# Kernel tuning notes

Measured on AMD Instinct MI355X. Metric: run time of the kernel, lower is better.

## Reference

```python
import jax, jax.numpy as jnp
import numpy as np

N = 50000      # nodes
D = 256        # input_features
K = 64         # hiddens (per-head out dim)
H = 8          # nheads
O = 64         # outputs
E = 1600000    # edges
ALPHA = 0.2    # leaky-relu negative slope


def setup_inputs() -> dict:
    key = jax.random.key(0)
    ks = jax.random.split(key, 8)
    x = jax.random.normal(ks[0], (N, D), dtype=jnp.float32)
    edges = jax.random.randint(ks[1], (2, E), 0, N, dtype=jnp.int64)
    layer_W = jax.random.normal(ks[2], (D, D), dtype=jnp.float32) * (1.0 / np.sqrt(D))
    layer_b = jnp.zeros((D,), dtype=jnp.float32)
    heads_W = jax.random.normal(ks[3], (H, D, K), dtype=jnp.float32) * (1.0 / np.sqrt(D))
    heads_a = jax.random.normal(ks[4], (H, 2 * K), dtype=jnp.float32) * 0.1
    end_W = jax.random.normal(ks[5], (H * K, O), dtype=jnp.float32) * (1.0 / np.sqrt(H * K))
    end_a = jax.random.normal(ks[6], (2 * O,), dtype=jnp.float32) * 0.1
    return {"x": x, "edges": edges, "layer_W": layer_W, "layer_b": layer_b,
            "heads_W": heads_W, "heads_a": heads_a, "end_W": end_W, "end_a": end_a}


def _gat_layer(x, W, a, src, dst):
    # x: [N, Din], W: [Din, Dout], a: [2*Dout]
    h = x @ W                                    # [N, Dout]
    k = h.shape[1]
    # a . [h_src || h_dst] == (h @ a_src)[src] + (h @ a_dst)[dst]  (cheap: project then gather scalars)
    s = (h @ a[:k])[src] + (h @ a[k:])[dst]      # [E]
    e = jax.nn.leaky_relu(s, ALPHA)
    # numerically-stable segment softmax over edges grouped by destination node
    m = jax.ops.segment_max(e, dst, num_segments=N)        # [N]
    w = jnp.exp(e - m[dst])                                # [E]
    denom = jax.ops.segment_sum(w, dst, num_segments=N)    # [N]
    attn = w / (denom[dst] + 1e-16)                        # [E]
    out = jax.ops.segment_sum(attn[:, None] * h[src], dst, num_segments=N)  # [N, Dout]
    return jax.nn.elu(out)


def reference(x, edges, layer_W, layer_b, heads_W, heads_a, end_W, end_a):
    src, dst = edges[0], edges[1]
    x = x @ layer_W + layer_b                    # nn.Linear(input_features, input_features)
    # multi-head sparse attention, concat over heads -> [N, H*K]
    hcat = jnp.concatenate(
        [_gat_layer(x, heads_W[i], heads_a[i], src, dst) for i in range(H)], axis=1)
    out = _gat_layer(hcat, end_W, end_a, src, dst)  # [N, O]
    return jax.nn.softmax(out, axis=1)
```

## Files before the change

kernel.cpp:

```cpp
#include <hip/hip_runtime.h>
#include <hip/hip_fp16.h>
#include <math.h>

#define NN 50000
#define DD 256
#define KK 64
#define HH 8
#define OO 64
#define EE 1600000
#define LRELU_ALPHA 0.2f
#define HK 512
#define NX 640
#define N3 80

typedef __attribute__((ext_vector_type(8))) short short8;
typedef __attribute__((ext_vector_type(4))) float floatx4;
typedef __attribute__((ext_vector_type(4))) unsigned int uintx4;

__device__ inline void bsplit(float f, unsigned short& h, unsigned short& l) {
    unsigned u = __float_as_uint(f);
    h = (unsigned short)(u >> 16);
    float fh = __uint_as_float(u & 0xffff0000u);
    l = (unsigned short)(__float_as_uint(f - fh) >> 16);
}

__device__ inline void fmamix2(float& a0, float& a1, unsigned int pk, float w) {
    asm("v_fma_mix_f32 %0, %2, %3, %0 op_sel:[0,0,0] op_sel_hi:[1,0,0]\n\t"
        "v_fma_mix_f32 %1, %2, %3, %1 op_sel:[1,0,0] op_sel_hi:[1,0,0]"
        : "+v"(a0), "+v"(a1)
        : "v"(pk), "v"(w));
}

__global__ void pack_heads_kernel(const float* __restrict__ hw, float* __restrict__ Bp) {
    int t = blockIdx.x * 256 + threadIdx.x;
    if (t >= HH * DD * KK) return;
    int h = t >> 14;
    int r = t & 16383;
    int d = r >> 6;
    int k = r & 63;
    Bp[d * HK + h * KK + k] = hw[t];
}

__global__ void bias_pack_kernel(const float* __restrict__ b, const float* __restrict__ Bp,
                                 float* __restrict__ bc) {
    int c = blockIdx.x * 256 + threadIdx.x;
    if (c >= HK) return;
    float s = 0.f;
    for (int d = 0; d < DD; d++) s += b[d] * Bp[d * HK + c];
    bc[c] = s;
}

__global__ void build_wext_kernel(const float* __restrict__ Wc, const float* __restrict__ heads_a,
                                  unsigned short* __restrict__ Th, unsigned short* __restrict__ Tl) {
    int t = blockIdx.x * 256 + threadIdx.x;
    int col = t >> 8, d = t & 255;
    if (col >= NX) return;
    float v = 0.f;
    if (col < HK) {
        v = Wc[d * HK + col];
    } else if (col < HK + 8) {
        int h = col - HK;
        for (int k = 0; k < 64; k++) v += Wc[d * HK + h * 64 + k] * heads_a[h * 128 + k];
    } else if (col < HK + 16) {
        int h = col - HK - 8;
        for (int k = 0; k < 64; k++) v += Wc[d * HK + h * 64 + k] * heads_a[h * 128 + 64 + k];
    }
    unsigned short hi, lo;
    bsplit(v, hi, lo);
    Th[(size_t)col * DD + d] = hi;
    Tl[(size_t)col * DD + d] = lo;
}

__global__ void bias_ext_kernel(const float* __restrict__ bc, const float* __restrict__ heads_a,
                                float* __restrict__ be) {
    int c = blockIdx.x * 256 + threadIdx.x;
    if (c >= NX) return;
    float v = 0.f;
    if (c < HK) v = bc[c];
    else if (c < HK + 8) {
        int h = c - HK;
        for (int k = 0; k < 64; k++) v += bc[h * 64 + k] * heads_a[h * 128 + k];
    } else if (c < HK + 16) {
        int h = c - HK - 8;
        for (int k = 0; k < 64; k++) v += bc[h * 64 + k] * heads_a[h * 128 + 64 + k];
    }
    be[c] = v;
}

__global__ void build_eext_kernel(const float* __restrict__ eW, const float* __restrict__ ea,
                                  unsigned short* __restrict__ Th, unsigned short* __restrict__ Tl) {
    int t = blockIdx.x * 256 + threadIdx.x;
    int col = t >> 9, k = t & 511;
    if (col >= N3) return;
    float v = 0.f;
    if (col < OO) v = eW[(size_t)k * OO + col];
    else if (col == OO) { for (int j = 0; j < OO; j++) v += eW[(size_t)k * OO + j] * ea[j]; }
    else if (col == OO + 1) { for (int j = 0; j < OO; j++) v += eW[(size_t)k * OO + j] * ea[64 + j]; }
    unsigned short hi, lo;
    bsplit(v, hi, lo);
    Th[(size_t)col * HK + k] = hi;
    Tl[(size_t)col * HK + k] = lo;
}

__global__ void split_x_kernel(const float* __restrict__ x, unsigned short* __restrict__ xh,
                               unsigned short* __restrict__ xl) {
    int t = blockIdx.x * 256 + threadIdx.x;
    if (t >= NN * 64) return;
    float4 v = ((const float4*)x)[t];
    ushort4 vh, vl;
    bsplit(v.x, vh.x, vl.x);
    bsplit(v.y, vh.y, vl.y);
    bsplit(v.z, vh.z, vl.z);
    bsplit(v.w, vh.w, vl.w);
    ((ushort4*)xh)[t] = vh;
    ((ushort4*)xl)[t] = vl;
}

#define GM 128
#define GN 128
#define GKT 16
__global__ __launch_bounds__(256) void sgemm128_kernel(
    const float* __restrict__ A, const float* __restrict__ B,
    const float* __restrict__ bias, float* __restrict__ C,
    int M, int N, int K)
{
    __shared__ float As[GKT][GM + 4];
    __shared__ float Bs[GKT][GN + 4];
    int tid = threadIdx.x;
    int row0 = blockIdx.y * GM, col0 = blockIdx.x * GN;
    int tx = tid & 15, ty = tid >> 4;
    int ar = tid >> 1;
    int ac0 = (tid & 1) * 8;
    float acc[8][8] = {};
    for (int k0 = 0; k0 < K; k0 += GKT) {
#pragma unroll
        for (int i = 0; i < 2; i++) {
            int gr = row0 + ar;
            int gc = k0 + ac0 + i * 4;
            float4 v = make_float4(0.f, 0.f, 0.f, 0.f);
            if (gr < M) v = *(const float4*)&A[(size_t)gr * K + gc];
            As[ac0 + i * 4 + 0][ar] = v.x;
            As[ac0 + i * 4 + 1][ar] = v.y;
            As[ac0 + i * 4 + 2][ar] = v.z;
            As[ac0 + i * 4 + 3][ar] = v.w;
        }
#pragma unroll
        for (int i = 0; i < 2; i++) {
            int idx = tid + i * 256;
            int br = idx >> 5;
            int bc = (idx & 31) * 4;
            float4 v = make_float4(0.f, 0.f, 0.f, 0.f);
            int gc = col0 + bc;
            if (gc < N) v = *(const float4*)&B[(size_t)(k0 + br) * N + gc];
            *(float4*)&Bs[br][bc] = v;
        }
        __syncthreads();
#pragma unroll
        for (int k = 0; k < GKT; k++) {
            float4 a0 = *(const float4*)&As[k][ty * 4];
            float4 a1 = *(const float4*)&As[k][64 + ty * 4];
            float4 b0 = *(const float4*)&Bs[k][tx * 4];
            float4 b1 = *(const float4*)&Bs[k][64 + tx * 4];
            float av[8] = {a0.x, a0.y, a0.z, a0.w, a1.x, a1.y, a1.z, a1.w};
            float bv[8] = {b0.x, b0.y, b0.z, b0.w, b1.x, b1.y, b1.z, b1.w};
#pragma unroll
            for (int i = 0; i < 8; i++)
#pragma unroll
                for (int j = 0; j < 8; j++) acc[i][j] += av[i] * bv[j];
        }
        __syncthreads();
    }
#pragma unroll
    for (int i = 0; i < 8; i++) {
        int gr = row0 + (i < 4 ? ty * 4 + i : 64 + ty * 4 + i - 4);
        if (gr >= M) continue;
#pragma unroll
        for (int j = 0; j < 8; j++) {
            int gc = col0 + (j < 4 ? tx * 4 + j : 64 + tx * 4 + j - 4);
            if (gc >= N) continue;
            float v = acc[i][j];
            if (bias) v += bias[gc];
            C[(size_t)gr * N + gc] = v;
        }
    }
}

#define LDA 40
__global__ __launch_bounds__(256) void mfma_gemm1_kernel(
    const unsigned short* __restrict__ xh, const unsigned short* __restrict__ xl,
    const unsigned short* __restrict__ BhT, const unsigned short* __restrict__ BlT,
    const float* __restrict__ bias_ext,
    __half* __restrict__ Hh_t, float* __restrict__ ssrc_t, float* __restrict__ sdst_t)
{
    __shared__ unsigned short AhL[128 * LDA];
    __shared__ unsigned short AlL[128 * LDA];
    __shared__ unsigned short BhL[128 * LDA];
    __shared__ unsigned short BlL[128 * LDA];
    int tid = threadIdx.x, widx = tid >> 6, lane = tid & 63;
    int row0 = blockIdx.y * 128, col0 = blockIdx.x * 128;
    int wrow = (widx >> 1) * 64, wcol = (widx & 1) * 64;
    int lrow = lane & 15, lq = lane >> 4;
    int sr = tid >> 1;
    int sc = (tid & 1) * 16;
    int gr = row0 + sr;
    size_t abase = (gr < NN) ? (size_t)gr * DD : 0;
    size_t bbase = (size_t)(col0 + sr) * DD;
    floatx4 acc[4][4] = {};
    uint4 pah0, pah1, pal0, pal1, pbh0, pbh1, pbl0, pbl1;
    {
        size_t ab = abase + sc, bb = bbase + sc;
        pah0 = *(const uint4*)&xh[ab];   pah1 = *(const uint4*)&xh[ab + 8];
        pal0 = *(const uint4*)&xl[ab];   pal1 = *(const uint4*)&xl[ab + 8];
        pbh0 = *(const uint4*)&BhT[bb];  pbh1 = *(const uint4*)&BhT[bb + 8];
        pbl0 = *(const uint4*)&BlT[bb];  pbl1 = *(const uint4*)&BlT[bb + 8];
    }
    for (int k0 = 0; k0 < DD; k0 += 32) {
        *(uint4*)&AhL[sr * LDA + sc]     = pah0;
        *(uint4*)&AhL[sr * LDA + sc + 8] = pah1;
        *(uint4*)&AlL[sr * LDA + sc]     = pal0;
        *(uint4*)&AlL[sr * LDA + sc + 8] = pal1;
        *(uint4*)&BhL[sr * LDA + sc]     = pbh0;
        *(uint4*)&BhL[sr * LDA + sc + 8] = pbh1;
        *(uint4*)&BlL[sr * LDA + sc]     = pbl0;
        *(uint4*)&BlL[sr * LDA + sc + 8] = pbl1;
        __syncthreads();
        if (k0 + 32 < DD) {
            size_t ab = abase + k0 + 32 + sc, bb = bbase + k0 + 32 + sc;
            pah0 = *(const uint4*)&xh[ab];   pah1 = *(const uint4*)&xh[ab + 8];
            pal0 = *(const uint4*)&xl[ab];   pal1 = *(const uint4*)&xl[ab + 8];
            pbh0 = *(const uint4*)&BhT[bb];  pbh1 = *(const uint4*)&BhT[bb + 8];
            pbl0 = *(const uint4*)&BlT[bb];  pbl1 = *(const uint4*)&BlT[bb + 8];
        }
        short8 ah[4], al[4], bh[4], bl[4];
#pragma unroll
        for (int mi = 0; mi < 4; mi++) {
            int r = wrow + mi * 16 + lrow;
            ah[mi] = *(const short8*)&AhL[r * LDA + lq * 8];
            al[mi] = *(const short8*)&AlL[r * LDA + lq * 8];
        }
#pragma unroll
        for (int ni = 0; ni < 4; ni++) {
            int c = wcol + ni * 16 + lrow;
            bh[ni] = *(const short8*)&BhL[c * LDA + lq * 8];
            bl[ni] = *(const short8*)&BlL[c * LDA + lq * 8];
        }
#pragma unroll
        for (int mi = 0; mi < 4; mi++)
#pragma unroll
            for (int ni = 0; ni < 4; ni++) {
                acc[mi][ni] = __builtin_amdgcn_mfma_f32_16x16x32_bf16(al[mi], bh[ni], acc[mi][ni], 0, 0, 0);
                acc[mi][ni] = __builtin_amdgcn_mfma_f32_16x16x32_bf16(ah[mi], bl[ni], acc[mi][ni], 0, 0, 0);
                acc[mi][ni] = __builtin_amdgcn_mfma_f32_16x16x32_bf16(ah[mi], bh[ni], acc[mi][ni], 0, 0, 0);
            }
        __syncthreads();
    }
#pragma unroll
    for (int mi = 0; mi < 4; mi++)
#pragma unroll
        for (int ni = 0; ni < 4; ni++)
#pragma unroll
            for (int r = 0; r < 4; r++) {
                int grow = row0 + wrow + mi * 16 + lq * 4 + r;
                int gcol = col0 + wcol + ni * 16 + lrow;
                if (grow < NN && gcol < HK + 16) {
                    float v = acc[mi][ni][r] + bias_ext[gcol];
                    if (gcol < HK)
                        Hh_t[((size_t)(gcol >> 6) * NN + grow) * 64 + (gcol & 63)] = __float2half_rn(v);
                    else if (gcol < HK + 8)
                        ssrc_t[(size_t)(gcol - HK) * NN + grow] = v;
                    else
                        sdst_t[(size_t)(gcol - HK - 8) * NN + grow] = v;
                }
            }
}

__global__ __launch_bounds__(256) void mfma_gemm3_kernel(
    const unsigned short* __restrict__ hch, const unsigned short* __restrict__ hcl,
    const unsigned short* __restrict__ BhT, const unsigned short* __restrict__ BlT,
    __half* __restrict__ h2, float* __restrict__ s2src, float* __restrict__ s2dst)
{
    __shared__ unsigned short AhL[64 * LDA];
    __shared__ unsigned short AlL[64 * LDA];
    __shared__ unsigned short BhL[N3 * LDA];
    __shared__ unsigned short BlL[N3 * LDA];
    int tid = threadIdx.x, widx = tid >> 6, lane = tid & 63;
    int row0 = blockIdx.x * 64;
    int wrow = widx * 16;
    int lrow = lane & 15, lq = lane >> 4;
    int sr = tid >> 2;
    int sc = (tid & 3) * 8;
    int gr = row0 + sr;
    size_t abase = (gr < NN) ? (size_t)gr * HK : 0;
    int bidx0 = tid;
    int br0 = bidx0 >> 2, bc0 = (bidx0 & 3) * 8;
    int bidx1 = tid + 256;
    bool b1ok = (bidx1 < N3 * 4);
    int br1 = bidx1 >> 2, bc1 = (bidx1 & 3) * 8;
    floatx4 acc[5] = {};
    uint4 pa0, pa1, pb0h, pb0l, pb1h, pb1l;
    {
        pa0 = *(const uint4*)&hch[abase + sc];
        pa1 = *(const uint4*)&hcl[abase + sc];
        pb0h = *(const uint4*)&BhT[(size_t)br0 * HK + bc0];
        pb0l = *(const uint4*)&BlT[(size_t)br0 * HK + bc0];
        if (b1ok) {
            pb1h = *(const uint4*)&BhT[(size_t)br1 * HK + bc1];
            pb1l = *(const uint4*)&BlT[(size_t)br1 * HK + bc1];
        }
    }
    for (int k0 = 0; k0 < HK; k0 += 32) {
        *(uint4*)&AhL[sr * LDA + sc] = pa0;
        *(uint4*)&AlL[sr * LDA + sc] = pa1;
        *(uint4*)&BhL[br0 * LDA + bc0] = pb0h;
        *(uint4*)&BlL[br0 * LDA + bc0] = pb0l;
        if (b1ok) {
            *(uint4*)&BhL[br1 * LDA + bc1] = pb1h;
            *(uint4*)&BlL[br1 * LDA + bc1] = pb1l;
        }
        __syncthreads();
        if (k0 + 32 < HK) {
            size_t ab = abase + k0 + 32 + sc;
            pa0 = *(const uint4*)&hch[ab];
            pa1 = *(const uint4*)&hcl[ab];
            pb0h = *(const uint4*)&BhT[(size_t)br0 * HK + k0 + 32 + bc0];
            pb0l = *(const uint4*)&BlT[(size_t)br0 * HK + k0 + 32 + bc0];
            if (b1ok) {
                pb1h = *(const uint4*)&BhT[(size_t)br1 * HK + k0 + 32 + bc1];
                pb1l = *(const uint4*)&BlT[(size_t)br1 * HK + k0 + 32 + bc1];
            }
        }
        short8 ah, al, bh[5], bl[5];
        int r = wrow + lrow;
        ah = *(const short8*)&AhL[r * LDA + lq * 8];
        al = *(const short8*)&AlL[r * LDA + lq * 8];
#pragma unroll
        for (int ni = 0; ni < 5; ni++) {
            int c = ni * 16 + lrow;
            bh[ni] = *(const short8*)&BhL[c * LDA + lq * 8];
            bl[ni] = *(const short8*)&BlL[c * LDA + lq * 8];
        }
#pragma unroll
        for (int ni = 0; ni < 5; ni++) {
            acc[ni] = __builtin_amdgcn_mfma_f32_16x16x32_bf16(al, bh[ni], acc[ni], 0, 0, 0);
            acc[ni] = __builtin_amdgcn_mfma_f32_16x16x32_bf16(ah, bl[ni], acc[ni], 0, 0, 0);
            acc[ni] = __builtin_amdgcn_mfma_f32_16x16x32_bf16(ah, bh[ni], acc[ni], 0, 0, 0);
        }
        __syncthreads();
    }
#pragma unroll
    for (int ni = 0; ni < 5; ni++)
#pragma unroll
        for (int r = 0; r < 4; r++) {
            int grow = row0 + wrow + lq * 4 + r;
            int gcol = ni * 16 + lrow;
            if (grow < NN) {
                float v = acc[ni][r];
                if (gcol < OO) h2[(size_t)grow * OO + gcol] = __float2half_rn(v);
                else if (gcol == OO) s2src[grow] = v;
                else if (gcol == OO + 1) s2dst[grow] = v;
            }
        }
}

__global__ void hist_kernel(const int* __restrict__ dst, int* __restrict__ deg) {
    int t = blockIdx.x * 256 + threadIdx.x;
    if (t < EE) atomicAdd(&deg[dst[t]], 1);
}

__global__ void scan1_kernel(const int* __restrict__ deg, int* __restrict__ part,
                             int* __restrict__ bsum) {
    __shared__ int ws_[4];
    int i = blockIdx.x * 256 + threadIdx.x;
    int lane = threadIdx.x & 63, wv = threadIdx.x >> 6;
    int v = (i < NN) ? deg[i] : 0;
    int x = v;
#pragma unroll
    for (int d = 1; d < 64; d <<= 1) {
        int t = __shfl_up(x, d, 64);
        if (lane >= d) x += t;
    }
    if (lane == 63) ws_[wv] = x;
    __syncthreads();
    int add = 0;
    for (int k = 0; k < wv; k++) add += ws_[k];
    x += add;
    if (i < NN) part[i] = x;
    if (threadIdx.x == 255) bsum[blockIdx.x] = x;
}

__global__ void scan2_kernel(int* __restrict__ bsum, int nb) {
    __shared__ int ws_[4];
    int tid = threadIdx.x;
    int lane = tid & 63, wv = tid >> 6;
    int v = (tid < nb) ? bsum[tid] : 0;
    int x = v;
#pragma unroll
    for (int d = 1; d < 64; d <<= 1) {
        int t = __shfl_up(x, d, 64);
        if (lane >= d) x += t;
    }
    if (lane == 63) ws_[wv] = x;
    __syncthreads();
    int add = 0;
    for (int k = 0; k < wv; k++) add += ws_[k];
    x += add;
    if (tid < nb) bsum[tid] = x;
}

__global__ void scan3_kernel(const int* __restrict__ deg, const int* __restrict__ part,
                             const int* __restrict__ bsum, int* __restrict__ offs,
                             int* __restrict__ cursor) {
    int i = blockIdx.x * 256 + threadIdx.x;
    if (i >= NN) return;
    int carry = blockIdx.x ? bsum[blockIdx.x - 1] : 0;
    int incl = part[i] + carry;
    offs[i + 1] = incl;
    cursor[i] = incl - deg[i];
    if (i == 0) offs[0] = 0;
}

__global__ void scatter_kernel(const int* __restrict__ src, const int* __restrict__ dst,
                               int* __restrict__ cursor, int* __restrict__ ssorted) {
    int t = blockIdx.x * 256 + threadIdx.x;
    if (t < EE) {
        int d = dst[t];
        int pos = atomicAdd(&cursor[d], 1);
        ssorted[pos] = src[t];
    }
}

#define APW 4
__global__ __launch_bounds__(256) void agg_heads_kernel(
    const __half* __restrict__ Hh_t, const float* __restrict__ ssrc_t,
    const float* __restrict__ sdst_t, const int* __restrict__ offs,
    const int* __restrict__ ssorted,
    unsigned short* __restrict__ hch, unsigned short* __restrict__ hcl)
{
    __shared__ int2 sSW[4][64];
    int wv = threadIdx.x >> 6, lane = threadIdx.x & 63;
    int w = blockIdx.x * 4 + wv;
    if (w >= NN * HH) return;
    int h = w / NN, n = w - h * NN;
    const __half* Hs = Hh_t + (size_t)h * NN * 64;
    const float* srcs = ssrc_t + (size_t)h * NN;
    int beg = offs[n], deg = offs[n + 1] - beg;
    int g = lane >> 3, q = lane & 7;
    float acc[8] = {};
    float den = 0.f;
    float sd = (deg > 0) ? sdst_t[(size_t)h * NN + n] : 0.f;
    for (int c0 = 0; c0 < deg; c0 += 64) {
        int jj = c0 + lane;
        int s = 0;
        float wgt = 0.f;
        if (jj < deg) {
            s = ssorted[beg + jj];
            float sv = srcs[s] + sd;
            float e = (sv >= 0.f) ? sv : LRELU_ALPHA * sv;
            wgt = __expf(e);
        }
        den += wgt;
        sSW[wv][lane] = make_int2(s, __float_as_int(wgt));
        int clen = min(64, deg - c0);
        int nst = (clen + 7) >> 3;
        for (int base = 0; base < nst; base += APW) {
            uint4 vb[APW];
            float wb[APW];
#pragma unroll
            for (int p2 = 0; p2 < APW; p2++) {
                int st = base + p2;
                int sj = 0;
                float ww = 0.f;
                if (st < nst) {
                    int2 t2 = sSW[wv][st * 8 + g];
                    sj = t2.x;
                    ww = __int_as_float(t2.y);
                }
                wb[p2] = ww;
                vb[p2] = *(const uint4*)&Hs[(size_t)sj * 64 + q * 8];
            }
#pragma unroll
            for (int p2 = 0; p2 < APW; p2++) {
                fmamix2(acc[0], acc[1], vb[p2].x, wb[p2]);
                fmamix2(acc[2], acc[3], vb[p2].y, wb[p2]);
                fmamix2(acc[4], acc[5], vb[p2].z, wb[p2]);
                fmamix2(acc[6], acc[7], vb[p2].w, wb[p2]);
            }
        }
    }
#pragma unroll
    for (int off = 32; off; off >>= 1) den += __shfl_xor(den, off, 64);
#pragma unroll
    for (int f = 0; f < 8; f++) {
        acc[f] += __shfl_xor(acc[f], 8, 64);
        acc[f] += __shfl_xor(acc[f], 16, 64);
        acc[f] += __shfl_xor(acc[f], 32, 64);
    }
    if (g == 0) {
        float inv = 1.f / (den + 1e-16f);
        unsigned int phw[4], plw[4];
#pragma unroll
        for (int j = 0; j < 4; j++) {
            float r0 = acc[2 * j] * inv, r1 = acc[2 * j + 1] * inv;
            r0 = (r0 > 0.f) ? r0 : (__expf(r0) - 1.f);
            r1 = (r1 > 0.f) ? r1 : (__expf(r1) - 1.f);
            unsigned short h0, l0, h1, l1;
            bsplit(r0, h0, l0);
            bsplit(r1, h1, l1);
            phw[j] = (unsigned)h0 | ((unsigned)h1 << 16);
            plw[j] = (unsigned)l0 | ((unsigned)l1 << 16);
        }
        size_t o = (size_t)n * HK + h * 64 + q * 8;
        uintx4 vph, vpl;
        vph.x = phw[0]; vph.y = phw[1]; vph.z = phw[2]; vph.w = phw[3];
        vpl.x = plw[0]; vpl.y = plw[1]; vpl.z = plw[2]; vpl.w = plw[3];
        __builtin_nontemporal_store(vph, (uintx4*)&hch[o]);
        __builtin_nontemporal_store(vpl, (uintx4*)&hcl[o]);
    }
}

__global__ __launch_bounds__(256) void agg_final_kernel(
    const __half* __restrict__ h2, const float* __restrict__ s2src,
    const float* __restrict__ s2dst, const int* __restrict__ offs,
    const int* __restrict__ ssorted, float* __restrict__ out)
{
    __shared__ int2 sSW[4][64];
    int wv = threadIdx.x >> 6, lane = threadIdx.x & 63;
    int n = blockIdx.x * 4 + wv;
    if (n >= NN) return;
    int beg = offs[n], deg = offs[n + 1] - beg;
    int g = lane >> 3, q = lane & 7;
    float acc[8] = {};
    float den = 0.f;
    float sd = (deg > 0) ? s2dst[n] : 0.f;
    for (int c0 = 0; c0 < deg; c0 += 64) {
        int jj = c0 + lane;
        int s = 0;
        float wgt = 0.f;
        if (jj < deg) {
            s = ssorted[beg + jj];
            float sv = s2src[s] + sd;
            float e = (sv >= 0.f) ? sv : LRELU_ALPHA * sv;
            wgt = __expf(e);
        }
        den += wgt;
        sSW[wv][lane] = make_int2(s, __float_as_int(wgt));
        int clen = min(64, deg - c0);
        int nst = (clen + 7) >> 3;
        for (int base = 0; base < nst; base += APW) {
            uint4 vb[APW];
            float wb[APW];
#pragma unroll
            for (int p2 = 0; p2 < APW; p2++) {
                int st = base + p2;
                int sj = 0;
                float ww = 0.f;
                if (st < nst) {
                    int2 t2 = sSW[wv][st * 8 + g];
                    sj = t2.x;
                    ww = __int_as_float(t2.y);
                }
                wb[p2] = ww;
                vb[p2] = *(const uint4*)&h2[(size_t)sj * OO + q * 8];
            }
#pragma unroll
            for (int p2 = 0; p2 < APW; p2++) {
                fmamix2(acc[0], acc[1], vb[p2].x, wb[p2]);
                fmamix2(acc[2], acc[3], vb[p2].y, wb[p2]);
                fmamix2(acc[4], acc[5], vb[p2].z, wb[p2]);
                fmamix2(acc[6], acc[7], vb[p2].w, wb[p2]);
            }
        }
    }
#pragma unroll
    for (int off = 32; off; off >>= 1) den += __shfl_xor(den, off, 64);
#pragma unroll
    for (int f = 0; f < 8; f++) {
        acc[f] += __shfl_xor(acc[f], 8, 64);
        acc[f] += __shfl_xor(acc[f], 16, 64);
        acc[f] += __shfl_xor(acc[f], 32, 64);
    }
    float inv = 1.f / (den + 1e-16f);
    float r[8];
#pragma unroll
    for (int f = 0; f < 8; f++) {
        float v = acc[f] * inv;
        r[f] = (v > 0.f) ? v : (__expf(v) - 1.f);
    }
    float mm = r[0];
#pragma unroll
    for (int f = 1; f < 8; f++) mm = fmaxf(mm, r[f]);
#pragma unroll
    for (int off = 1; off < 8; off <<= 1) mm = fmaxf(mm, __shfl_xor(mm, off, 64));
    float p[8], sum = 0.f;
#pragma unroll
    for (int f = 0; f < 8; f++) { p[f] = __expf(r[f] - mm); sum += p[f]; }
#pragma unroll
    for (int off = 1; off < 8; off <<= 1) sum += __shfl_xor(sum, off, 64);
    float is = 1.f / sum;
    if (g == 0) {
        float4 o0 = make_float4(p[0] * is, p[1] * is, p[2] * is, p[3] * is);
        float4 o1 = make_float4(p[4] * is, p[5] * is, p[6] * is, p[7] * is);
        *(float4*)&out[(size_t)n * OO + q * 8] = o0;
        *(float4*)&out[(size_t)n * OO + q * 8 + 4] = o1;
    }
}

extern "C" void kernel_launch(void* const* d_in, const int* in_sizes, int n_in,
                              void* d_out, int out_size, void* d_ws, size_t ws_size,
                              hipStream_t stream) {
    const float* x       = (const float*)d_in[0];
    const int*   edges   = (const int*)d_in[1];
    const float* layer_W = (const float*)d_in[2];
    const float* layer_b = (const float*)d_in[3];
    const float* heads_W = (const float*)d_in[4];
    const float* heads_a = (const float*)d_in[5];
    const float* end_W   = (const float*)d_in[6];
    const float* end_a   = (const float*)d_in[7];
    float* out = (float*)d_out;

    const int* src = edges;
    const int* dst = edges + EE;

    char* ws = (char*)d_ws;
    size_t wsp = 0;
    auto alloc = [&](size_t bytes) -> void* {
        void* r = ws + wsp;
        wsp += (bytes + 255) & ~(size_t)255;
        return r;
    };
    __half* Hh_t  = (__half*)alloc((size_t)NN * HK * 2);
    unsigned short* hch = (unsigned short*)alloc((size_t)NN * HK * 2);
    unsigned short* hcl = (unsigned short*)alloc((size_t)NN * HK * 2);
    __half* h2    = (__half*)alloc((size_t)NN * OO * 2);
    float* Bp    = (float*)alloc((size_t)DD * HK * 4);
    float* Wc    = (float*)alloc((size_t)DD * HK * 4);
    float* bc    = (float*)alloc((size_t)HK * 4);
    unsigned short* WexthT = (unsigned short*)alloc((size_t)NX * DD * 2);
    unsigned short* WextlT = (unsigned short*)alloc((size_t)NX * DD * 2);
    unsigned short* eexthT = (unsigned short*)alloc((size_t)N3 * HK * 2);
    unsigned short* eextlT = (unsigned short*)alloc((size_t)N3 * HK * 2);
    float* bias_ext = (float*)alloc((size_t)NX * 4);
    float* ssrc_t = (float*)alloc((size_t)HH * NN * 4);
    float* sdst_t = (float*)alloc((size_t)HH * NN * 4);
    float* s2src = (float*)alloc((size_t)NN * 4);
    float* s2dst = (float*)alloc((size_t)NN * 4);
    int* deg     = (int*)alloc((size_t)NN * 4);
    int* offs    = (int*)alloc((size_t)(NN + 1) * 4);
    int* cursor  = (int*)alloc((size_t)NN * 4);
    int* part    = (int*)alloc((size_t)NN * 4);
    int* bsum    = (int*)alloc((size_t)256 * 4);
    int* ssorted = (int*)alloc((size_t)EE * 4);

    unsigned short* xh = hch;
    unsigned short* xl = hcl;

    const int NB = (NN + 255) / 256;

    (void)hipMemsetAsync(deg, 0, (size_t)NN * 4, stream);

    pack_heads_kernel<<<(HH * DD * KK + 255) / 256, 256, 0, stream>>>(heads_W, Bp);
    bias_pack_kernel<<<2, 256, 0, stream>>>(layer_b, Bp, bc);
    sgemm128_kernel<<<dim3(HK / GN, DD / GM), 256, 0, stream>>>(
        layer_W, Bp, nullptr, Wc, DD, HK, DD);
    build_wext_kernel<<<(NX * DD + 255) / 256, 256, 0, stream>>>(Wc, heads_a, WexthT, WextlT);
    bias_ext_kernel<<<(NX + 255) / 256, 256, 0, stream>>>(bc, heads_a, bias_ext);
    build_eext_kernel<<<(N3 * HK + 255) / 256, 256, 0, stream>>>(end_W, end_a, eexthT, eextlT);
    split_x_kernel<<<(NN * 64 + 255) / 256, 256, 0, stream>>>(x, xh, xl);

    mfma_gemm1_kernel<<<dim3(NX / 128, (NN + 127) / 128), 256, 0, stream>>>(
        xh, xl, WexthT, WextlT, bias_ext, Hh_t, ssrc_t, sdst_t);

    hist_kernel<<<(EE + 255) / 256, 256, 0, stream>>>(dst, deg);
    scan1_kernel<<<NB, 256, 0, stream>>>(deg, part, bsum);
    scan2_kernel<<<1, 256, 0, stream>>>(bsum, NB);
    scan3_kernel<<<NB, 256, 0, stream>>>(deg, part, bsum, offs, cursor);
    scatter_kernel<<<(EE + 255) / 256, 256, 0, stream>>>(src, dst, cursor, ssorted);

    agg_heads_kernel<<<(NN * HH + 3) / 4, 256, 0, stream>>>(
        Hh_t, ssrc_t, sdst_t, offs, ssorted, hch, hcl);

    mfma_gemm3_kernel<<<(NN + 63) / 64, 256, 0, stream>>>(
        hch, hcl, eexthT, eextlT, h2, s2src, s2dst);

    agg_final_kernel<<<(NN + 3) / 4, 256, 0, stream>>>(h2, s2src, s2dst, offs, ssorted, out);
}
```

Measured before the change: 776.9 us.

## Switch head features to node-major layout and aggregate all heads per wave

The first GEMM now writes head features and attention scores node-major, so all 8 heads of a node sit next to each other. The head aggregation kernel now uses one wavefront per node instead of one per (head, node). Each lane computes the edge weight for one (edge, head) pair, and each gathered source row is a contiguous 1 KB read covering all heads. The goal is to cut redundant index loads and scattered per-head gathers. In exchange, the kernel takes more loop iterations with only 8 edges per chunk and has less wave-level parallelism.

```diff
diff --git a/kernel.cpp b/kernel.cpp
--- a/kernel.cpp
+++ b/kernel.cpp
@@ -190,7 +190,7 @@
     const unsigned short* __restrict__ xh, const unsigned short* __restrict__ xl,
     const unsigned short* __restrict__ BhT, const unsigned short* __restrict__ BlT,
     const float* __restrict__ bias_ext,
-    __half* __restrict__ Hh_t, float* __restrict__ ssrc_t, float* __restrict__ sdst_t)
+    __half* __restrict__ Hh, float* __restrict__ ssrc_n, float* __restrict__ sdst_n)
 {
     __shared__ unsigned short AhL[128 * LDA];
     __shared__ unsigned short AlL[128 * LDA];
@@ -265,11 +265,11 @@
                 if (grow < NN && gcol < HK + 16) {
                     float v = acc[mi][ni][r] + bias_ext[gcol];
                     if (gcol < HK)
-                        Hh_t[((size_t)(gcol >> 6) * NN + grow) * 64 + (gcol & 63)] = __float2half_rn(v);
+                        Hh[(size_t)grow * HK + gcol] = __float2half_rn(v);
                     else if (gcol < HK + 8)
-                        ssrc_t[(size_t)(gcol - HK) * NN + grow] = v;
+                        ssrc_n[(size_t)grow * 8 + (gcol - HK)] = v;
                     else
-                        sdst_t[(size_t)(gcol - HK - 8) * NN + grow] = v;
+                        sdst_n[(size_t)grow * 8 + (gcol - HK - 8)] = v;
                 }
             }
 }
@@ -429,95 +429,81 @@
     }
 }
 
-#define APW 4
+#define APE 4
 __global__ __launch_bounds__(256) void agg_heads_kernel(
-    const __half* __restrict__ Hh_t, const float* __restrict__ ssrc_t,
-    const float* __restrict__ sdst_t, const int* __restrict__ offs,
+    const __half* __restrict__ Hh, const float* __restrict__ ssrc_n,
+    const float* __restrict__ sdst_n, const int* __restrict__ offs,
     const int* __restrict__ ssorted,
     unsigned short* __restrict__ hch, unsigned short* __restrict__ hcl)
 {
     __shared__ int2 sSW[4][64];
     int wv = threadIdx.x >> 6, lane = threadIdx.x & 63;
-    int w = blockIdx.x * 4 + wv;
-    if (w >= NN * HH) return;
-    int h = w / NN, n = w - h * NN;
-    const __half* Hs = Hh_t + (size_t)h * NN * 64;
-    const float* srcs = ssrc_t + (size_t)h * NN;
+    int n = blockIdx.x * 4 + wv;
+    if (n >= NN) return;
     int beg = offs[n], deg = offs[n + 1] - beg;
-    int g = lane >> 3, q = lane & 7;
+    int eg = lane >> 3, hh = lane & 7;
     float acc[8] = {};
     float den = 0.f;
-    float sd = (deg > 0) ? sdst_t[(size_t)h * NN + n] : 0.f;
-    for (int c0 = 0; c0 < deg; c0 += 64) {
-        int jj = c0 + lane;
+    float sd = sdst_n[(size_t)n * 8 + hh];
+    for (int c0 = 0; c0 < deg; c0 += 8) {
+        int jj = c0 + eg;
         int s = 0;
         float wgt = 0.f;
         if (jj < deg) {
             s = ssorted[beg + jj];
-            float sv = srcs[s] + sd;
+            float sv = ssrc_n[(size_t)s * 8 + hh] + sd;
             float e = (sv >= 0.f) ? sv : LRELU_ALPHA * sv;
             wgt = __expf(e);
         }
         den += wgt;
         sSW[wv][lane] = make_int2(s, __float_as_int(wgt));
-        int clen = min(64, deg - c0);
-        int nst = (clen + 7) >> 3;
-        for (int base = 0; base < nst; base += APW) {
-            uint4 vb[APW];
-            float wb[APW];
-#pragma unroll
-            for (int p2 = 0; p2 < APW; p2++) {
-                int st = base + p2;
-                int sj = 0;
-                float ww = 0.f;
-                if (st < nst) {
-                    int2 t2 = sSW[wv][st * 8 + g];
-                    sj = t2.x;
-                    ww = __int_as_float(t2.y);
-                }
-                wb[p2] = ww;
-                vb[p2] = *(const uint4*)&Hs[(size_t)sj * 64 + q * 8];
-            }
-#pragma unroll
-            for (int p2 = 0; p2 < APW; p2++) {
-                fmamix2(acc[0], acc[1], vb[p2].x, wb[p2]);
-                fmamix2(acc[2], acc[3], vb[p2].y, wb[p2]);
-                fmamix2(acc[4], acc[5], vb[p2].z, wb[p2]);
-                fmamix2(acc[6], acc[7], vb[p2].w, wb[p2]);
-            }
-        }
-    }
-#pragma unroll
-    for (int off = 32; off; off >>= 1) den += __shfl_xor(den, off, 64);
-#pragma unroll
-    for (int f = 0; f < 8; f++) {
-        acc[f] += __shfl_xor(acc[f], 8, 64);
-        acc[f] += __shfl_xor(acc[f], 16, 64);
-        acc[f] += __shfl_xor(acc[f], 32, 64);
-    }
-    if (g == 0) {
-        float inv = 1.f / (den + 1e-16f);
-        unsigned int phw[4], plw[4];
-#pragma unroll
-        for (int j = 0; j < 4; j++) {
-            float r0 = acc[2 * j] * inv, r1 = acc[2 * j + 1] * inv;
-            r0 = (r0 > 0.f) ? r0 : (__expf(r0) - 1.f);
-            r1 = (r1 > 0.f) ? r1 : (__expf(r1) - 1.f);
-            unsigned short h0, l0, h1, l1;
-            bsplit(r0, h0, l0);
-            bsplit(r1, h1, l1);
-            phw[j] = (unsigned)h0 | ((unsigned)h1 << 16);
-            plw[j] = (unsigned)l0 | ((unsigned)l1 << 16);
-        }
-        size_t o = (size_t)n * HK + h * 64 + q * 8;
-        uintx4 vph, vpl;
-        vph.x = phw[0]; vph.y = phw[1]; vph.z = phw[2]; vph.w = phw[3];
-        vpl.x = plw[0]; vpl.y = plw[1]; vpl.z = plw[2]; vpl.w = plw[3];
-        __builtin_nontemporal_store(vph, (uintx4*)&hch[o]);
-        __builtin_nontemporal_store(vpl, (uintx4*)&hcl[o]);
-    }
-}
-
+        int ec = min(8, deg - c0);
+#pragma unroll
+        for (int base = 0; base < 8; base += APE) {
+            if (base >= ec) break;
+            uint4 vb[APE];
+            float wb[APE];
+#pragma unroll
+            for (int p = 0; p < APE; p++) {
+                int2 t2 = sSW[wv][(base + p) * 8 + (lane >> 3)];
+                wb[p] = __int_as_float(t2.y);
+                vb[p] = *(const uint4*)&Hh[((size_t)t2.x << 9) + lane * 8];
+            }
+#pragma unroll
+            for (int p = 0; p < APE; p++) {
+                fmamix2(acc[0], acc[1], vb[p].x, wb[p]);
+                fmamix2(acc[2], acc[3], vb[p].y, wb[p]);
+                fmamix2(acc[4], acc[5], vb[p].z, wb[p]);
+                fmamix2(acc[6], acc[7], vb[p].w, wb[p]);
+            }
+        }
+    }
+    den += __shfl_xor(den, 8, 64);
+    den += __shfl_xor(den, 16, 64);
+    den += __shfl_xor(den, 32, 64);
+    float denf = __shfl(den, lane >> 3, 64);
+    float inv = 1.f / (denf + 1e-16f);
+    unsigned int phw[4], plw[4];
+#pragma unroll
+    for (int j = 0; j < 4; j++) {
+        float r0 = acc[2 * j] * inv, r1 = acc[2 * j + 1] * inv;
+        r0 = (r0 > 0.f) ? r0 : (__expf(r0) - 1.f);
+        r1 = (r1 > 0.f) ? r1 : (__expf(r1) - 1.f);
+        unsigned short h0, l0, h1, l1;
+        bsplit(r0, h0, l0);
+        bsplit(r1, h1, l1);
+        phw[j] = (unsigned)h0 | ((unsigned)h1 << 16);
+        plw[j] = (unsigned)l0 | ((unsigned)l1 << 16);
+    }
+    size_t o = (size_t)n * HK + lane * 8;
+    uintx4 vph, vpl;
+    vph.x = phw[0]; vph.y = phw[1]; vph.z = phw[2]; vph.w = phw[3];
+    vpl.x = plw[0]; vpl.y = plw[1]; vpl.z = plw[2]; vpl.w = plw[3];
+    __builtin_nontemporal_store(vph, (uintx4*)&hch[o]);
+    __builtin_nontemporal_store(vpl, (uintx4*)&hcl[o]);
+}
+
+#define APW 4
 __global__ __launch_bounds__(256) void agg_final_kernel(
     const __half* __restrict__ h2, const float* __restrict__ s2src,
     const float* __restrict__ s2dst, const int* __restrict__ offs,
@@ -628,7 +614,7 @@
         wsp += (bytes + 255) & ~(size_t)255;
         return r;
     };
-    __half* Hh_t  = (__half*)alloc((size_t)NN * HK * 2);
+    __half* Hh    = (__half*)alloc((size_t)NN * HK * 2);
     unsigned short* hch = (unsigned short*)alloc((size_t)NN * HK * 2);
     unsigned short* hcl = (unsigned short*)alloc((size_t)NN * HK * 2);
     __half* h2    = (__half*)alloc((size_t)NN * OO * 2);
@@ -640,8 +626,8 @@
     unsigned short* eexthT = (unsigned short*)alloc((size_t)N3 * HK * 2);
     unsigned short* eextlT = (unsigned short*)alloc((size_t)N3 * HK * 2);
     float* bias_ext = (float*)alloc((size_t)NX * 4);
-    float* ssrc_t = (float*)alloc((size_t)HH * NN * 4);
-    float* sdst_t = (float*)alloc((size_t)HH * NN * 4);
+    float* ssrc_n = (float*)alloc((size_t)NN * 8 * 4);
+    float* sdst_n = (float*)alloc((size_t)NN * 8 * 4);
     float* s2src = (float*)alloc((size_t)NN * 4);
     float* s2dst = (float*)alloc((size_t)NN * 4);
     int* deg     = (int*)alloc((size_t)NN * 4);
@@ -668,7 +654,7 @@
     split_x_kernel<<<(NN * 64 + 255) / 256, 256, 0, stream>>>(x, xh, xl);
 
     mfma_gemm1_kernel<<<dim3(NX / 128, (NN + 127) / 128), 256, 0, stream>>>(
-        xh, xl, WexthT, WextlT, bias_ext, Hh_t, ssrc_t, sdst_t);
+        xh, xl, WexthT, WextlT, bias_ext, Hh, ssrc_n, sdst_n);
 
     hist_kernel<<<(EE + 255) / 256, 256, 0, stream>>>(dst, deg);
     scan1_kernel<<<NB, 256, 0, stream>>>(deg, part, bsum);
@@ -676,8 +662,8 @@
     scan3_kernel<<<NB, 256, 0, stream>>>(deg, part, bsum, offs, cursor);
     scatter_kernel<<<(EE + 255) / 256, 256, 0, stream>>>(src, dst, cursor, ssorted);
 
-    agg_heads_kernel<<<(NN * HH + 3) / 4, 256, 0, stream>>>(
-        Hh_t, ssrc_t, sdst_t, offs, ssorted, hch, hcl);
+    agg_heads_kernel<<<(NN + 3) / 4, 256, 0, stream>>>(
+        Hh, ssrc_n, sdst_n, offs, ssorted, hch, hcl);
 
     mfma_gemm3_kernel<<<(NN + 63) / 64, 256, 0, stream>>>(
         hch, hcl, eexthT, eextlT, h2, s2src, s2dst);
```

After: 802.5 us. 1.03x slower.
